# Performance work log

Measured on AMD Instinct MI355X. Metric: run time of the kernel, lower is better.

## Reference

```python
import jax, jax.numpy as jnp
import numpy as np

N_NODES = 100000
N_EDGES = 1600000
IN_DIM, HID_DIM, OUT_DIM = 128, 64, 64
NEG_SLOPE = 0.2


def _gat_layer(h_in, src, dst, W, a_src, a_dst, b, n_nodes):
    # h: [N, F_out]
    h = h_in @ W.T
    alpha_src = h @ a_src  # [N]
    alpha_dst = h @ a_dst  # [N]
    # per-edge raw attention logits (edge j->i: src=j, dst=i)
    e = jax.nn.leaky_relu(alpha_src[src] + alpha_dst[dst], NEG_SLOPE)  # [E]
    # segment softmax over incoming edges of each dst node
    m = jax.ops.segment_max(e, dst, num_segments=n_nodes)
    ex = jnp.exp(e - m[dst])
    denom = jax.ops.segment_sum(ex, dst, num_segments=n_nodes)
    alpha = ex / denom[dst]  # [E], denom > 0 thanks to self-loops
    out = jax.ops.segment_sum(h[src] * alpha[:, None], dst, num_segments=n_nodes)
    return out + b


def setup_inputs() -> dict:
    key = jax.random.key(0)
    ks = jax.random.split(key, 12)
    x = jax.random.normal(ks[0], (N_NODES, IN_DIM), dtype=jnp.float32)
    edge_index = jax.random.randint(ks[1], (2, N_EDGES), 0, N_NODES)
    edge_attr = jax.random.normal(ks[2], (N_EDGES, 1), dtype=jnp.float32)
    s1 = 1.0 / np.sqrt(IN_DIM)
    s2 = 1.0 / np.sqrt(HID_DIM)
    W1 = jax.random.normal(ks[3], (HID_DIM, IN_DIM), dtype=jnp.float32) * s1
    att_src1 = jax.random.normal(ks[4], (HID_DIM,), dtype=jnp.float32) * s2
    att_dst1 = jax.random.normal(ks[5], (HID_DIM,), dtype=jnp.float32) * s2
    b1 = jnp.zeros((HID_DIM,), dtype=jnp.float32)
    W2 = jax.random.normal(ks[6], (OUT_DIM, HID_DIM), dtype=jnp.float32) * s2
    att_src2 = jax.random.normal(ks[7], (OUT_DIM,), dtype=jnp.float32) * s2
    att_dst2 = jax.random.normal(ks[8], (OUT_DIM,), dtype=jnp.float32) * s2
    b2 = jnp.zeros((OUT_DIM,), dtype=jnp.float32)
    return {"x": x, "edge_index": edge_index, "edge_attr": edge_attr,
            "W1": W1, "att_src1": att_src1, "att_dst1": att_dst1, "b1": b1,
            "W2": W2, "att_src2": att_src2, "att_dst2": att_dst2, "b2": b2}


def reference(x, edge_index, edge_attr, W1, att_src1, att_dst1, b1,
              W2, att_src2, att_dst2, b2):
    n = x.shape[0]
    # add self-loops (PyG GATConv default); edge_attr unused (edge_dim=None)
    loop = jnp.arange(n, dtype=edge_index.dtype)
    src = jnp.concatenate([edge_index[0], loop])
    dst = jnp.concatenate([edge_index[1], loop])
    h = _gat_layer(x, src, dst, W1, att_src1, att_dst1, b1, n)
    h = jax.nn.relu(h)
    h = _gat_layer(h, src, dst, W2, att_src2, att_dst2, b2, n)
    # global_mean_pool with batch=None -> mean over all nodes, shape [1, F]
    return jnp.mean(h, axis=0, keepdims=True)
```

## Files before the change

### kernel.cpp

```cpp
#include <hip/hip_runtime.h>

#define NEG_SLOPE 0.2f
#define BSHIFT 6
#define NBMAX 2048
#define BCAP 1408
#define CHUNK 4096

__device__ __forceinline__ unsigned short f2b(float x) {
    unsigned u = __float_as_uint(x);
    u += 0x7fff + ((u >> 16) & 1);
    return (unsigned short)(u >> 16);
}
__device__ __forceinline__ float b2f(unsigned short u) {
    return __uint_as_float((unsigned)u << 16);
}

__global__ __launch_bounds__(256) void hist_kernel(
    const int* __restrict__ ei, int* __restrict__ hist, int E, int NB)
{
    __shared__ int cnt[NBMAX];
    const int tid = threadIdx.x;
    for (int i = tid; i < NB; i += 256) cnt[i] = 0;
    __syncthreads();
    const int start = blockIdx.x * CHUNK;
    const int end = min(start + CHUNK, E);
    for (int i = start + tid; i < end; i += 256)
        atomicAdd(&cnt[ei[E + i] >> BSHIFT], 1);
    __syncthreads();
    for (int i = tid; i < NB; i += 256)
        hist[(size_t)blockIdx.x * NB + i] = cnt[i];
}

__global__ __launch_bounds__(256) void colscan_kernel(
    int* __restrict__ hist, int* __restrict__ btotal, int NB, int NBLK)
{
    const int b = blockIdx.x * 256 + threadIdx.x;
    if (b >= NB) return;
    int run = 0;
    int blk = 0;
    for (; blk + 8 <= NBLK; blk += 8) {
        int w[8];
        #pragma unroll
        for (int j = 0; j < 8; ++j) w[j] = hist[(size_t)(blk + j) * NB + b];
        #pragma unroll
        for (int j = 0; j < 8; ++j) {
            hist[(size_t)(blk + j) * NB + b] = run;
            run += w[j];
        }
    }
    for (; blk < NBLK; ++blk) {
        int w = hist[(size_t)blk * NB + b];
        hist[(size_t)blk * NB + b] = run;
        run += w;
    }
    btotal[b] = run;
}

__global__ __launch_bounds__(256) void scatter_kernel(
    const int* __restrict__ ei, const int* __restrict__ hist,
    int* __restrict__ binned, int E, int NB)
{
    __shared__ int base[NBMAX], cnt2[NBMAX];
    const int tid = threadIdx.x;
    for (int i = tid; i < NB; i += 256) {
        base[i] = hist[(size_t)blockIdx.x * NB + i];
        cnt2[i] = 0;
    }
    __syncthreads();
    const int start = blockIdx.x * CHUNK;
    const int end = min(start + CHUNK, E);
    for (int i = start + tid; i < end; i += 256) {
        int s = ei[i], d = ei[E + i];
        int b = d >> BSHIFT;
        int r = base[b] + atomicAdd(&cnt2[b], 1);
        if (r < BCAP) binned[(size_t)b * BCAP + r] = (s << BSHIFT) | (d & 63);
    }
}

__global__ __launch_bounds__(256) void bscan_kernel(
    const int* __restrict__ btotal, int* __restrict__ bbase, int NB)
{
    __shared__ int lds[256];
    const int t = threadIdx.x;
    int v[8]; int s = 0;
    #pragma unroll
    for (int j = 0; j < 8; ++j) {
        int i = t * 8 + j;
        v[j] = (i < NB) ? min(btotal[i], BCAP) : 0;
        s += v[j];
    }
    lds[t] = s;
    __syncthreads();
    #pragma unroll
    for (int off = 1; off < 256; off <<= 1) {
        int x = (t >= off) ? lds[t - off] : 0;
        __syncthreads();
        lds[t] += x;
        __syncthreads();
    }
    int excl = (t > 0) ? lds[t - 1] : 0;
    #pragma unroll
    for (int j = 0; j < 8; ++j) {
        int i = t * 8 + j;
        if (i < NB) { bbase[i] = excl + 64 * i; excl += v[j]; }
    }
}

__global__ __launch_bounds__(256) void bucket_csr_kernel(
    const int* __restrict__ binned, const int* __restrict__ btotal,
    const int* __restrict__ bbase, int* __restrict__ row_ptr,
    int* __restrict__ esrc, int N)
{
    __shared__ int ldeg[64];
    __shared__ int lcur[64];
    const int b = blockIdx.x;
    const int tid = threadIdx.x;
    const int node0 = b << BSHIFT;
    const int cnt = min(btotal[b], BCAP);
    const int base_e = bbase[b];
    const int* bp = binned + (size_t)b * BCAP;

    if (tid < 64) ldeg[tid] = (node0 + tid < N) ? 1 : 0;
    __syncthreads();
    for (int i = tid; i < cnt; i += 256)
        atomicAdd(&ldeg[bp[i] & 63], 1);
    __syncthreads();
    if (tid < 64) {
        int v = ldeg[tid];
        int inc = v;
        #pragma unroll
        for (int off = 1; off < 64; off <<= 1) {
            int t2 = __shfl_up(inc, off, 64);
            if (tid >= off) inc += t2;
        }
        int excl = inc - v;
        int node = node0 + tid;
        if (node <= N) row_ptr[node] = base_e + excl;
        if (node < N) {
            esrc[base_e + excl] = node;
            lcur[tid] = base_e + excl + 1;
        }
    }
    __syncthreads();
    for (int i = tid; i < cnt; i += 256) {
        int v = bp[i];
        int pos = atomicAdd(&lcur[v & 63], 1);
        esrc[pos] = v >> BSHIFT;
    }
}

template<int K>
__global__ __launch_bounds__(256) void gemm_attn_kernel(
    const float* __restrict__ in, const float* __restrict__ W,
    const float* __restrict__ a_src, const float* __restrict__ a_dst,
    unsigned short* __restrict__ hb, float* __restrict__ asrc,
    float* __restrict__ adst, int N)
{
    constexpr int KB = 64;
    constexpr int NKC = KB / 4;
    constexpr int LDN = 65;
    __shared__ float4 xs4[NKC * LDN];
    __shared__ float4 ws4[NKC * LDN];
    __shared__ float avs[64], avd[64];

    const int tid = threadIdx.x;
    const int node0 = blockIdx.x * 64;
    const int tf = tid & 15;
    const int tn = tid >> 4;

    if (tid < 64) { avs[tid] = a_src[tid]; avd[tid] = a_dst[tid]; }

    float acc[4][4] = {};

    for (int k0 = 0; k0 < K; k0 += KB) {
        if (k0) __syncthreads();
        for (int i = tid; i < 64 * NKC; i += 256) {
            int r = i >> 4, kc = i & 15;
            int node = node0 + r;
            float4 xv = (node < N)
                ? *(const float4*)&in[(size_t)node * K + k0 + 4 * kc]
                : make_float4(0.f, 0.f, 0.f, 0.f);
            xs4[kc * LDN + r] = xv;
            ws4[kc * LDN + r] = *(const float4*)&W[(size_t)r * K + k0 + 4 * kc];
        }
        __syncthreads();

        #pragma unroll 4
        for (int kc = 0; kc < NKC; ++kc) {
            float4 xv[4], wv[4];
            #pragma unroll
            for (int i = 0; i < 4; ++i) xv[i] = xs4[kc * LDN + 4 * tn + i];
            #pragma unroll
            for (int j = 0; j < 4; ++j) wv[j] = ws4[kc * LDN + tf + 16 * j];
            #pragma unroll
            for (int i = 0; i < 4; ++i)
                #pragma unroll
                for (int j = 0; j < 4; ++j) {
                    acc[i][j] = fmaf(xv[i].x, wv[j].x, acc[i][j]);
                    acc[i][j] = fmaf(xv[i].y, wv[j].y, acc[i][j]);
                    acc[i][j] = fmaf(xv[i].z, wv[j].z, acc[i][j]);
                    acc[i][j] = fmaf(xv[i].w, wv[j].w, acc[i][j]);
                }
        }
    }

    #pragma unroll
    for (int i = 0; i < 4; ++i) {
        const int node = node0 + 4 * tn + i;
        const bool valid = node < N;
        float vs = 0.f, vd = 0.f;
        #pragma unroll
        for (int j = 0; j < 4; ++j) {
            int f = tf + 16 * j;
            if (valid) hb[(size_t)node * 64 + f] = f2b(acc[i][j]);
            vs = fmaf(acc[i][j], avs[f], vs);
            vd = fmaf(acc[i][j], avd[f], vd);
        }
        #pragma unroll
        for (int off = 8; off >= 1; off >>= 1) {
            vs += __shfl_down(vs, off, 16);
            vd += __shfl_down(vd, off, 16);
        }
        if (tf == 0 && valid) { asrc[node] = vs; adst[node] = vd; }
    }
}

__global__ __launch_bounds__(256) void aggregate_csr_kernel(
    const int* __restrict__ row_ptr, const int* __restrict__ esrc,
    const float* __restrict__ asrc, const float* __restrict__ adst,
    const unsigned short* __restrict__ hb, const float* __restrict__ bias,
    float* __restrict__ g, int N, int do_relu)
{
    const int node = (int)((blockIdx.x * 256 + threadIdx.x) >> 4);
    const int lane = threadIdx.x & 15;
    if (node >= N) return;
    const int beg = row_ptr[node];
    const int end = row_ptr[node + 1];
    const float ad = adst[node];
    float a0 = 0.f, a1 = 0.f, a2 = 0.f, a3 = 0.f, wsum = 0.f;
    int p = beg;
    for (; p + 4 <= end; p += 4) {
        int s[4]; ushort4 r[4]; float l[4];
        #pragma unroll
        for (int j = 0; j < 4; ++j) s[j] = esrc[p + j];
        #pragma unroll
        for (int j = 0; j < 4; ++j)
            r[j] = *(const ushort4*)(hb + (size_t)s[j] * 64 + lane * 4);
        #pragma unroll
        for (int j = 0; j < 4; ++j) l[j] = asrc[s[j]] + ad;
        #pragma unroll
        for (int j = 0; j < 4; ++j) {
            float ll = (l[j] > 0.f) ? l[j] : NEG_SLOPE * l[j];
            float w = __expf(ll);
            wsum += w;
            a0 = fmaf(w, b2f(r[j].x), a0);
            a1 = fmaf(w, b2f(r[j].y), a1);
            a2 = fmaf(w, b2f(r[j].z), a2);
            a3 = fmaf(w, b2f(r[j].w), a3);
        }
    }
    for (; p < end; ++p) {
        int s = esrc[p];
        ushort4 r = *(const ushort4*)(hb + (size_t)s * 64 + lane * 4);
        float l = asrc[s] + ad;
        l = (l > 0.f) ? l : NEG_SLOPE * l;
        float w = __expf(l);
        wsum += w;
        a0 = fmaf(w, b2f(r.x), a0);
        a1 = fmaf(w, b2f(r.y), a1);
        a2 = fmaf(w, b2f(r.z), a2);
        a3 = fmaf(w, b2f(r.w), a3);
    }
    const float inv = 1.0f / wsum;
    float4 v = make_float4(a0 * inv, a1 * inv, a2 * inv, a3 * inv);
    if (bias) {
        v.x += bias[lane * 4 + 0]; v.y += bias[lane * 4 + 1];
        v.z += bias[lane * 4 + 2]; v.w += bias[lane * 4 + 3];
    }
    if (do_relu) {
        v.x = fmaxf(v.x, 0.f); v.y = fmaxf(v.y, 0.f);
        v.z = fmaxf(v.z, 0.f); v.w = fmaxf(v.w, 0.f);
    }
    *(float4*)&g[(size_t)node * 64 + lane * 4] = v;
}

__global__ __launch_bounds__(256) void pool_kernel(
    const float* __restrict__ g, const float* __restrict__ b2,
    float* __restrict__ out, int N)
{
    __shared__ float red[256];
    const int f = threadIdx.x & 63;
    const int sub = threadIdx.x >> 6;
    float acc = 0.f;
    for (int n = blockIdx.x * 4 + sub; n < N; n += gridDim.x * 4)
        acc += g[(size_t)n * 64 + f];
    red[threadIdx.x] = acc;
    __syncthreads();
    if (threadIdx.x < 64) {
        float s = red[f] + red[64 + f] + red[128 + f] + red[192 + f];
        atomicAdd(out + f, s * (1.0f / (float)N));
        if (blockIdx.x == 0) atomicAdd(out + f, b2[f]);
    }
}

extern "C" void kernel_launch(void* const* d_in, const int* in_sizes, int n_in,
                              void* d_out, int out_size, void* d_ws, size_t ws_size,
                              hipStream_t stream) {
    const float* x   = (const float*)d_in[0];
    const int*   ei  = (const int*)d_in[1];
    const float* W1  = (const float*)d_in[3];
    const float* as1 = (const float*)d_in[4];
    const float* ad1 = (const float*)d_in[5];
    const float* b1  = (const float*)d_in[6];
    const float* W2  = (const float*)d_in[7];
    const float* as2 = (const float*)d_in[8];
    const float* ad2 = (const float*)d_in[9];
    const float* b2  = (const float*)d_in[10];
    float* out = (float*)d_out;

    const int N = in_sizes[0] / 128;
    const int E = in_sizes[1] / 2;
    const int Etot = E + N;
    const int NB = (N + 63) >> BSHIFT;
    const int NBLK = (E + CHUNK - 1) / CHUNK;

    auto align4 = [](size_t v) { return (v + 3) & ~(size_t)3; };
    float* ws    = (float*)d_ws;
    size_t off = 0;
    unsigned short* hb = (unsigned short*)(ws + off); off += align4((size_t)N * 32);
    float* g     = ws + off; off += align4((size_t)N * 64);
    float* asrc  = ws + off; off += align4(N);
    float* adst  = ws + off; off += align4(N);
    int* row_ptr = (int*)(ws + off); off += align4(N + 1);
    int* btotal  = (int*)(ws + off); off += NBMAX;
    int* bbase   = (int*)(ws + off); off += NBMAX;
    int* hist    = (int*)(ws + off); off += align4((size_t)NBLK * NB);
    int* esrc    = (int*)(ws + off); off += align4(Etot);
    int* binned  = (int*)g;

    const int gemm_blocks = (N + 63) / 64;
    const int agg_blocks  = (int)(((size_t)N * 16 + 255) / 256);

    hipMemsetAsync(out, 0, 64 * sizeof(float), stream);

    hist_kernel<<<NBLK, 256, 0, stream>>>(ei, hist, E, NB);
    colscan_kernel<<<(NB + 255) / 256, 256, 0, stream>>>(hist, btotal, NB, NBLK);
    scatter_kernel<<<NBLK, 256, 0, stream>>>(ei, hist, binned, E, NB);
    bscan_kernel<<<1, 256, 0, stream>>>(btotal, bbase, NB);
    bucket_csr_kernel<<<NB, 256, 0, stream>>>(binned, btotal, bbase, row_ptr, esrc, N);

    gemm_attn_kernel<128><<<gemm_blocks, 256, 0, stream>>>(x, W1, as1, ad1, hb, asrc, adst, N);
    aggregate_csr_kernel<<<agg_blocks, 256, 0, stream>>>(row_ptr, esrc, asrc, adst, hb, b1, g, N, 1);

    gemm_attn_kernel<64><<<gemm_blocks, 256, 0, stream>>>(g, W2, as2, ad2, hb, asrc, adst, N);
    aggregate_csr_kernel<<<agg_blocks, 256, 0, stream>>>(row_ptr, esrc, asrc, adst, hb, nullptr, g, N, 0);

    pool_kernel<<<512, 256, 0, stream>>>(g, b2, out, N);
}
```

Measured before the change: 319.0 us.

## Use bf16 MFMA for node GEMMs and store hidden features in bf16

Replaces the FP32 FMA register-tiled GEMM with bf16 MFMA 16x16x32 instructions. Inputs and weights are converted to bf16 in shared memory, and K is loaded in one pass instead of KB chunks. The aggregate kernel now writes the intermediate features as bf16, so the second GEMM and the pool kernel read half as many bytes. The cost is lower precision in the first-layer inputs and the stored activations, plus a larger shared-memory footprint per block.

```diff
diff --git a/kernel.cpp b/kernel.cpp
--- a/kernel.cpp
+++ b/kernel.cpp
@@ -5,6 +5,9 @@
 #define NBMAX 2048
 #define BCAP 1408
 #define CHUNK 4096
+
+typedef __attribute__((ext_vector_type(8))) short short8;
+typedef __attribute__((ext_vector_type(4))) float f32x4;
 
 __device__ __forceinline__ unsigned short f2b(float x) {
     unsigned u = __float_as_uint(x);
@@ -149,79 +152,86 @@
     }
 }
 
-template<int K>
+template<int K, bool BF16IN>
 __global__ __launch_bounds__(256) void gemm_attn_kernel(
-    const float* __restrict__ in, const float* __restrict__ W,
+    const void* __restrict__ in_v, const float* __restrict__ W,
     const float* __restrict__ a_src, const float* __restrict__ a_dst,
     unsigned short* __restrict__ hb, float* __restrict__ asrc,
     float* __restrict__ adst, int N)
 {
-    constexpr int KB = 64;
-    constexpr int NKC = KB / 4;
-    constexpr int LDN = 65;
-    __shared__ float4 xs4[NKC * LDN];
-    __shared__ float4 ws4[NKC * LDN];
+    constexpr int LDK = K + 8;
+    __shared__ unsigned short xb[64 * LDK];
+    __shared__ unsigned short wb[64 * LDK];
     __shared__ float avs[64], avd[64];
 
     const int tid = threadIdx.x;
     const int node0 = blockIdx.x * 64;
-    const int tf = tid & 15;
-    const int tn = tid >> 4;
+    const int w = tid >> 6;
+    const int lane = tid & 63;
+    const int col = lane & 15;
+    const int quad = lane >> 4;
 
     if (tid < 64) { avs[tid] = a_src[tid]; avd[tid] = a_dst[tid]; }
 
-    float acc[4][4] = {};
-
-    for (int k0 = 0; k0 < K; k0 += KB) {
-        if (k0) __syncthreads();
-        for (int i = tid; i < 64 * NKC; i += 256) {
-            int r = i >> 4, kc = i & 15;
+    for (int i = tid; i < 64 * (K / 4); i += 256) {
+        int r = i / (K / 4), c = i % (K / 4);
+        float4 v = *(const float4*)&W[(size_t)r * K + 4 * c];
+        *(ushort4*)&wb[r * LDK + 4 * c] =
+            make_ushort4(f2b(v.x), f2b(v.y), f2b(v.z), f2b(v.w));
+    }
+    if (BF16IN) {
+        const unsigned short* in = (const unsigned short*)in_v;
+        for (int i = tid; i < 64 * (K / 8); i += 256) {
+            int r = i / (K / 8), c = i % (K / 8);
             int node = node0 + r;
-            float4 xv = (node < N)
-                ? *(const float4*)&in[(size_t)node * K + k0 + 4 * kc]
-                : make_float4(0.f, 0.f, 0.f, 0.f);
-            xs4[kc * LDN + r] = xv;
-            ws4[kc * LDN + r] = *(const float4*)&W[(size_t)r * K + k0 + 4 * kc];
-        }
-        __syncthreads();
-
-        #pragma unroll 4
-        for (int kc = 0; kc < NKC; ++kc) {
-            float4 xv[4], wv[4];
-            #pragma unroll
-            for (int i = 0; i < 4; ++i) xv[i] = xs4[kc * LDN + 4 * tn + i];
-            #pragma unroll
-            for (int j = 0; j < 4; ++j) wv[j] = ws4[kc * LDN + tf + 16 * j];
-            #pragma unroll
-            for (int i = 0; i < 4; ++i)
-                #pragma unroll
-                for (int j = 0; j < 4; ++j) {
-                    acc[i][j] = fmaf(xv[i].x, wv[j].x, acc[i][j]);
-                    acc[i][j] = fmaf(xv[i].y, wv[j].y, acc[i][j]);
-                    acc[i][j] = fmaf(xv[i].z, wv[j].z, acc[i][j]);
-                    acc[i][j] = fmaf(xv[i].w, wv[j].w, acc[i][j]);
-                }
-        }
-    }
-
-    #pragma unroll
-    for (int i = 0; i < 4; ++i) {
-        const int node = node0 + 4 * tn + i;
+            ulonglong2 v = (node < N)
+                ? *(const ulonglong2*)&in[(size_t)node * K + 8 * c]
+                : make_ulonglong2(0ull, 0ull);
+            *(ulonglong2*)&xb[r * LDK + 8 * c] = v;
+        }
+    } else {
+        const float* in = (const float*)in_v;
+        for (int i = tid; i < 64 * (K / 4); i += 256) {
+            int r = i / (K / 4), c = i % (K / 4);
+            int node = node0 + r;
+            float4 v = (node < N) ? *(const float4*)&in[(size_t)node * K + 4 * c]
+                                  : make_float4(0.f, 0.f, 0.f, 0.f);
+            *(ushort4*)&xb[r * LDK + 4 * c] =
+                make_ushort4(f2b(v.x), f2b(v.y), f2b(v.z), f2b(v.w));
+        }
+    }
+    __syncthreads();
+
+    f32x4 acc[4] = {f32x4{0,0,0,0}, f32x4{0,0,0,0}, f32x4{0,0,0,0}, f32x4{0,0,0,0}};
+    #pragma unroll
+    for (int kc = 0; kc < K / 32; ++kc) {
+        short8 a = *(const short8*)&xb[(16 * w + col) * LDK + kc * 32 + quad * 8];
+        #pragma unroll
+        for (int j = 0; j < 4; ++j) {
+            short8 b = *(const short8*)&wb[(16 * j + col) * LDK + kc * 32 + quad * 8];
+            acc[j] = __builtin_amdgcn_mfma_f32_16x16x32_bf16(a, b, acc[j], 0, 0, 0);
+        }
+    }
+
+    #pragma unroll
+    for (int r = 0; r < 4; ++r) {
+        const int node = node0 + 16 * w + quad * 4 + r;
         const bool valid = node < N;
         float vs = 0.f, vd = 0.f;
         #pragma unroll
         for (int j = 0; j < 4; ++j) {
-            int f = tf + 16 * j;
-            if (valid) hb[(size_t)node * 64 + f] = f2b(acc[i][j]);
-            vs = fmaf(acc[i][j], avs[f], vs);
-            vd = fmaf(acc[i][j], avd[f], vd);
+            float hv = acc[j][r];
+            int f = 16 * j + col;
+            if (valid) hb[(size_t)node * 64 + f] = f2b(hv);
+            vs = fmaf(hv, avs[f], vs);
+            vd = fmaf(hv, avd[f], vd);
         }
         #pragma unroll
         for (int off = 8; off >= 1; off >>= 1) {
             vs += __shfl_down(vs, off, 16);
             vd += __shfl_down(vd, off, 16);
         }
-        if (tf == 0 && valid) { asrc[node] = vs; adst[node] = vd; }
+        if (col == 0 && valid) { asrc[node] = vs; adst[node] = vd; }
     }
 }
 
@@ -229,7 +239,7 @@
     const int* __restrict__ row_ptr, const int* __restrict__ esrc,
     const float* __restrict__ asrc, const float* __restrict__ adst,
     const unsigned short* __restrict__ hb, const float* __restrict__ bias,
-    float* __restrict__ g, int N, int do_relu)
+    unsigned short* __restrict__ gb, int N, int do_relu)
 {
     const int node = (int)((blockIdx.x * 256 + threadIdx.x) >> 4);
     const int lane = threadIdx.x & 15;
@@ -281,11 +291,12 @@
         v.x = fmaxf(v.x, 0.f); v.y = fmaxf(v.y, 0.f);
         v.z = fmaxf(v.z, 0.f); v.w = fmaxf(v.w, 0.f);
     }
-    *(float4*)&g[(size_t)node * 64 + lane * 4] = v;
+    *(ushort4*)&gb[(size_t)node * 64 + lane * 4] =
+        make_ushort4(f2b(v.x), f2b(v.y), f2b(v.z), f2b(v.w));
 }
 
 __global__ __launch_bounds__(256) void pool_kernel(
-    const float* __restrict__ g, const float* __restrict__ b2,
+    const unsigned short* __restrict__ gb, const float* __restrict__ b2,
     float* __restrict__ out, int N)
 {
     __shared__ float red[256];
@@ -293,7 +304,7 @@
     const int sub = threadIdx.x >> 6;
     float acc = 0.f;
     for (int n = blockIdx.x * 4 + sub; n < N; n += gridDim.x * 4)
-        acc += g[(size_t)n * 64 + f];
+        acc += b2f(gb[(size_t)n * 64 + f]);
     red[threadIdx.x] = acc;
     __syncthreads();
     if (threadIdx.x < 64) {
@@ -328,7 +339,7 @@
     float* ws    = (float*)d_ws;
     size_t off = 0;
     unsigned short* hb = (unsigned short*)(ws + off); off += align4((size_t)N * 32);
-    float* g     = ws + off; off += align4((size_t)N * 64);
+    unsigned short* gb = (unsigned short*)(ws + off); off += align4((size_t)N * 32);
     float* asrc  = ws + off; off += align4(N);
     float* adst  = ws + off; off += align4(N);
     int* row_ptr = (int*)(ws + off); off += align4(N + 1);
@@ -336,7 +347,7 @@
     int* bbase   = (int*)(ws + off); off += NBMAX;
     int* hist    = (int*)(ws + off); off += align4((size_t)NBLK * NB);
     int* esrc    = (int*)(ws + off); off += align4(Etot);
-    int* binned  = (int*)g;
+    int* binned  = (int*)gb;
 
     const int gemm_blocks = (N + 63) / 64;
     const int agg_blocks  = (int)(((size_t)N * 16 + 255) / 256);
@@ -349,11 +360,15 @@
     bscan_kernel<<<1, 256, 0, stream>>>(btotal, bbase, NB);
     bucket_csr_kernel<<<NB, 256, 0, stream>>>(binned, btotal, bbase, row_ptr, esrc, N);
 
-    gemm_attn_kernel<128><<<gemm_blocks, 256, 0, stream>>>(x, W1, as1, ad1, hb, asrc, adst, N);
-    aggregate_csr_kernel<<<agg_blocks, 256, 0, stream>>>(row_ptr, esrc, asrc, adst, hb, b1, g, N, 1);
-
-    gemm_attn_kernel<64><<<gemm_blocks, 256, 0, stream>>>(g, W2, as2, ad2, hb, asrc, adst, N);
-    aggregate_csr_kernel<<<agg_blocks, 256, 0, stream>>>(row_ptr, esrc, asrc, adst, hb, nullptr, g, N, 0);
-
-    pool_kernel<<<512, 256, 0, stream>>>(g, b2, out, N);
-}
+    gemm_attn_kernel<128, false><<<gemm_blocks, 256, 0, stream>>>(
+        x, W1, as1, ad1, hb, asrc, adst, N);
+    aggregate_csr_kernel<<<agg_blocks, 256, 0, stream>>>(
+        row_ptr, esrc, asrc, adst, hb, b1, gb, N, 1);
+
+    gemm_attn_kernel<64, true><<<gemm_blocks, 256, 0, stream>>>(
+        gb, W2, as2, ad2, hb, asrc, adst, N);
+    aggregate_csr_kernel<<<agg_blocks, 256, 0, stream>>>(
+        row_ptr, esrc, asrc, adst, hb, nullptr, gb, N, 0);
+
+    pool_kernel<<<512, 256, 0, stream>>>(gb, b2, out, N);
+}
```

Measured after the change: 298.4 us. -6.4%, faster.
